# Kernel tuning notes

Measured on AMD Instinct MI355X. Metric: run time of the kernel, lower is better.

The kernel has to match this reference:

```python
import jax, jax.numpy as jnp
from jax import lax
import numpy as np

B, S, T = 64, 256, 256          # sentences, tokens, parser transitions per sentence
WDIMS, PDIMS = 128, 32
H = 256                          # per-direction hidden = ldims // 2
LDIMS = 2 * H
HID = 512
NRELS = 46
K, NNVECS = 3, 3
SLOTS = (K + 1) * NNVECS         # 12 gathered hidden vectors per transition
FEAT = LDIMS * SLOTS             # 6144 = hidLayer input dim
VW, VP = 40003, 53
ROUT = 2 * NRELS + 1             # 93


def _lstm(x, Wih, Whh, bih, bhh, reverse=False):
    """torch.nn.LSTMCell recurrence over seq axis. x: [B,S,D] -> h: [B,S,H]."""
    Bx = x.shape[0]
    Hh = Whh.shape[1]
    xs = jnp.swapaxes(x, 0, 1)  # [S,B,D]
    xg = xs @ Wih.T + (bih + bhh)  # precompute input gates [S,B,4H]

    def step(carry, g_in):
        h, c = carry
        g = g_in + h @ Whh.T
        i, f, gg, o = jnp.split(g, 4, axis=-1)
        i = jax.nn.sigmoid(i); f = jax.nn.sigmoid(f)
        gg = jnp.tanh(gg); o = jax.nn.sigmoid(o)
        c = f * c + i * gg
        h = o * jnp.tanh(c)
        return (h, c), h

    init = (jnp.zeros((Bx, Hh), x.dtype), jnp.zeros((Bx, Hh), x.dtype))
    _, hs = lax.scan(step, init, xg, reverse=reverse)
    return jnp.swapaxes(hs, 0, 1)  # [B,S,H], backward pass aligned to positions


def _forward(word_ids, pos_ids, feat_idx, wlookup, plookup,
             Wih1f, Whh1f, bih1f, bhh1f, Wih1b, Whh1b, bih1b, bhh1b,
             Wih2f, Whh2f, bih2f, bhh2f, Wih2b, Whh2b, bih2b, bhh2b,
             hidLayer, hidBias, outLayer, outBias,
             rhidLayer, rhidBias, routLayer, routBias):
    # token embeddings: ivec = cat(wordvec, posvec)
    ivec = jnp.concatenate([wlookup[word_ids], plookup[pos_ids]], axis=-1)  # [B,S,160]
    # first biLSTM
    f1 = _lstm(ivec, Wih1f, Whh1f, bih1f, bhh1f)
    b1 = _lstm(ivec, Wih1b, Whh1b, bih1b, bhh1b, reverse=True)
    vec1 = jnp.concatenate([f1, b1], axis=-1)  # [B,S,512]
    # second biLSTM (bibiFlag)
    f2 = _lstm(vec1, Wih2f, Whh2f, bih2f, bhh2f)
    b2 = _lstm(vec1, Wih2b, Whh2b, bih2b, bhh2b, reverse=True)
    vec = jnp.concatenate([f2, b2], axis=-1)  # [B,S,512]
    # __evaluate: concat (k+1)*nnvecs hidden vectors per transition
    bidx = jnp.arange(B)[:, None, None]
    feats = vec[bidx, feat_idx]                      # [B,T,12,512]
    feats = feats.reshape(B, T, FEAT)                # [B,T,6144]
    # unlabeled action scores: out = outLayer @ tanh(hidLayer @ input + hidBias) + outBias
    hid = jnp.tanh(jnp.einsum('btf,hf->bth', feats, hidLayer) + hidBias)
    out = jnp.einsum('bth,oh->bto', hid, outLayer) + outBias        # [B,T,3]
    # labeled relation scores
    rhid = jnp.tanh(jnp.einsum('btf,hf->bth', feats, rhidLayer) + rhidBias)
    rout = jnp.einsum('bth,oh->bto', rhid, routLayer) + routBias    # [B,T,93]
    return out, rout


def setup_inputs() -> dict:
    key = jax.random.key(0)
    ks = iter(jax.random.split(key, 40))

    def nrm(shape, scale=0.05):
        return jax.random.normal(next(ks), shape, jnp.float32) * scale

    inp = {}
    inp['word_ids'] = jax.random.randint(next(ks), (B, S), 0, VW)
    inp['pos_ids'] = jax.random.randint(next(ks), (B, S), 0, VP)
    inp['feat_idx'] = jax.random.randint(next(ks), (B, T, SLOTS), 0, S)
    inp['wlookup'] = nrm((VW, WDIMS))
    inp['plookup'] = nrm((VP, PDIMS))
    D1 = WDIMS + PDIMS
    for tag, din in (('1f', D1), ('1b', D1), ('2f', LDIMS), ('2b', LDIMS)):
        inp['Wih' + tag] = nrm((4 * H, din))
        inp['Whh' + tag] = nrm((4 * H, H))
        inp['bih' + tag] = nrm((4 * H,))
        inp['bhh' + tag] = nrm((4 * H,))
    inp['hidLayer'] = nrm((HID, FEAT), 0.02)
    inp['hidBias'] = nrm((HID,))
    inp['outLayer'] = nrm((3, HID))
    inp['outBias'] = nrm((3,))
    inp['rhidLayer'] = nrm((HID, FEAT), 0.02)
    inp['rhidBias'] = nrm((HID,))
    inp['routLayer'] = nrm((ROUT, HID))
    inp['routBias'] = nrm((ROUT,))
    return inp


def reference(word_ids, pos_ids, feat_idx, wlookup, plookup,
              Wih1f, Whh1f, bih1f, bhh1f, Wih1b, Whh1b, bih1b, bhh1b,
              Wih2f, Whh2f, bih2f, bhh2f, Wih2b, Whh2b, bih2b, bhh2b,
              hidLayer, hidBias, outLayer, outBias,
              rhidLayer, rhidBias, routLayer, routBias):
    return _forward(word_ids, pos_ids, feat_idx, wlookup, plookup,
                    Wih1f, Whh1f, bih1f, bhh1f, Wih1b, Whh1b, bih1b, bhh1b,
                    Wih2f, Whh2f, bih2f, bhh2f, Wih2b, Whh2b, bih2b, bhh2b,
                    hidLayer, hidBias, outLayer, outBias,
                    rhidLayer, rhidBias, routLayer, routBias)
```

## Files before the change

### kernel.cpp

```cpp
#include <hip/hip_runtime.h>
#include <hip/hip_fp16.h>
#include <math.h>


namespace {
constexpr int kB = 64, kS = 256, kH = 256, kG4 = 1024;
constexpr int kLD = 512;
constexpr int kTok = kB * kS;
}

typedef _Float16 h2 __attribute__((ext_vector_type(2)));
typedef _Float16 h4 __attribute__((ext_vector_type(4)));
typedef _Float16 h8 __attribute__((ext_vector_type(8)));
typedef float f4 __attribute__((ext_vector_type(4)));

#if __has_builtin(__builtin_amdgcn_fdot2)
#define USE_FDOT2 1
#else
#define USE_FDOT2 0
#endif

__device__ __forceinline__ float dot2acc(h2 w, h2 hh, float acc) {
#if USE_FDOT2
  return __builtin_amdgcn_fdot2(w, hh, acc, false);
#else
  return fmaf((float)w.x, (float)hh.x, fmaf((float)w.y, (float)hh.y, acc));
#endif
}

__device__ __forceinline__ float fastrcp(float x) {
#if __has_builtin(__builtin_amdgcn_rcpf)
  return __builtin_amdgcn_rcpf(x);
#else
  return 1.f / x;
#endif
}
__device__ __forceinline__ float sigf(float x) { return fastrcp(1.f + __expf(-x)); }
__device__ __forceinline__ float tanhfast(float x) {
  float u = __expf(2.f * x);
  return 1.f - 2.f * fastrcp(u + 1.f);
}

__device__ __forceinline__ void stage16(const void* g, void* lds_base, int lane) {
#if __has_builtin(__builtin_amdgcn_global_load_lds)
  (void)lane;
  __builtin_amdgcn_global_load_lds((const __attribute__((address_space(1))) void*)g,
                                   (__attribute__((address_space(3))) void*)lds_base,
                                   16, 0, 0);
#else
  *(uint4*)((char*)lds_base + lane * 16) = *(const uint4*)g;
#endif
}

__global__ void embed_h(const int* __restrict__ wid, const int* __restrict__ pid,
                        const float* __restrict__ wl, const float* __restrict__ pl,
                        _Float16* __restrict__ dst) {
  int tid = blockIdx.x * blockDim.x + threadIdx.x;
  if (tid >= kTok * 24) return;
  int tok = tid / 24, c8 = tid % 24;
  h8 o;
  if (c8 < 20) {
    const float* src = (c8 < 16) ? (wl + (size_t)wid[tok] * 128 + c8 * 8)
                                 : (pl + (size_t)pid[tok] * 32 + (c8 - 16) * 8);
    float4 v0 = *(const float4*)src;
    float4 v1 = *(const float4*)(src + 4);
    o[0] = (_Float16)v0.x; o[1] = (_Float16)v0.y;
    o[2] = (_Float16)v0.z; o[3] = (_Float16)v0.w;
    o[4] = (_Float16)v1.x; o[5] = (_Float16)v1.y;
    o[6] = (_Float16)v1.z; o[7] = (_Float16)v1.w;
  } else {
    o = (h8)(_Float16)0.f;
  }
  *(h8*)(dst + (size_t)tok * 192 + c8 * 8) = o;
}

__global__ void f2h_pad(const float* __restrict__ src, _Float16* __restrict__ dst,
                        int rows, int Kin, int Kpad) {
  int per = Kpad >> 2;
  int tid = blockIdx.x * blockDim.x + threadIdx.x;
  if (tid >= rows * per) return;
  int row = tid / per, c4 = (tid % per) << 2;
  h4 o;
  if (c4 < Kin) {
    float4 v = *(const float4*)(src + (size_t)row * Kin + c4);
    o[0] = (_Float16)v.x; o[1] = (_Float16)v.y;
    o[2] = (_Float16)v.z; o[3] = (_Float16)v.w;
  } else {
    o = (h4)(_Float16)0.f;
  }
  *(h4*)(dst + (size_t)row * Kpad + c4) = o;
}

__global__ void prep_bias(const float* __restrict__ b0, const float* __restrict__ b1,
                          const float* __restrict__ b2, const float* __restrict__ b3,
                          const float* __restrict__ b4, const float* __restrict__ b5,
                          const float* __restrict__ b6, const float* __restrict__ b7,
                          float* __restrict__ bsum) {
  int tid = blockIdx.x * blockDim.x + threadIdx.x;
  if (tid >= 4 * kG4) return;
  int grp = tid >> 10, i = tid & 1023;
  const float* x; const float* y;
  switch (grp) {
    case 0: x = b0; y = b1; break;
    case 1: x = b2; y = b3; break;
    case 2: x = b4; y = b5; break;
    default: x = b6; y = b7; break;
  }
  bsum[tid] = x[i] + y[i];
}

__global__ void concat_bias(const float* __restrict__ a, const float* __restrict__ b,
                            float* __restrict__ dst) {
  int tid = blockIdx.x * blockDim.x + threadIdx.x;
  if (tid >= kG4) return;
  dst[tid] = (tid < 512) ? a[tid] : b[tid - 512];
}

template <bool GATHER, bool TANH>
__global__ __launch_bounds__(256) void mfma_gemm(
    const _Float16* __restrict__ A, int lda,
    const _Float16* __restrict__ W,
    const float* __restrict__ bias,
    const _Float16* __restrict__ vsrc, const int* __restrict__ fidx,
    float* __restrict__ C, int K) {
  __shared__ _Float16 Asm[128 * 64];
  __shared__ _Float16 Bsm[128 * 64];
  const int tid = threadIdx.x;
  const int w = tid >> 6, l = tid & 63;
  const int wr = w >> 1, wc = w & 1;
  const int m0 = blockIdx.y * 128, n0 = blockIdx.x * 128;
  const int lrow = l & 15, lk8 = (l >> 4) << 3;
  const int stg_r = l >> 3;
  const int stg_c = (l & 7) ^ stg_r;

  f4 acc[4][4] = {};

  for (int k0 = 0; k0 < K; k0 += 64) {
#pragma unroll
    for (int ii = 0; ii < 4; ++ii) {
      const int r = w * 32 + ii * 8 + stg_r;
      const _Float16* ga;
      if (GATHER) {
        const int token = m0 + r;
        const int slot = k0 >> 9;
        const int idx = fidx[token * 12 + slot];
        ga = vsrc + ((((size_t)(token >> 8) << 8) + idx) << 9) + (k0 & 511) + (stg_c << 3);
      } else {
        ga = A + (size_t)(m0 + r) * lda + k0 + (stg_c << 3);
      }
      stage16(ga, &Asm[(size_t)(w * 32 + ii * 8) * 64], l);
      const _Float16* gb = W + (size_t)(n0 + r) * K + k0 + (stg_c << 3);
      stage16(gb, &Bsm[(size_t)(w * 32 + ii * 8) * 64], l);
    }
    __syncthreads();
#pragma unroll
    for (int kk = 0; kk < 64; kk += 32) {
      const int c0 = (kk + lk8) >> 3;
      h8 af[4], bf[4];
#pragma unroll
      for (int m = 0; m < 4; ++m) {
        const int row = wr * 64 + m * 16 + lrow;
        af[m] = *(const h8*)&Asm[row * 64 + ((c0 ^ (row & 7)) << 3)];
      }
#pragma unroll
      for (int n = 0; n < 4; ++n) {
        const int row = wc * 64 + n * 16 + lrow;
        bf[n] = *(const h8*)&Bsm[row * 64 + ((c0 ^ (row & 7)) << 3)];
      }
#pragma unroll
      for (int m = 0; m < 4; ++m)
#pragma unroll
        for (int n = 0; n < 4; ++n)
          acc[m][n] = __builtin_amdgcn_mfma_f32_16x16x32_f16(af[m], bf[n], acc[m][n], 0, 0, 0);
    }
    __syncthreads();
  }
#pragma unroll
  for (int n = 0; n < 4; ++n) {
    const int col = n0 + wc * 64 + n * 16 + lrow;
    const float bb = bias[col];
#pragma unroll
    for (int m = 0; m < 4; ++m) {
      const int rowb = m0 + wr * 64 + m * 16 + ((l >> 4) << 2);
#pragma unroll
      for (int r = 0; r < 4; ++r) {
        float v = acc[m][n][r] + bb;
        if (TANH) v = tanhf(v);
        C[(size_t)(rowb + r) * kG4 + col] = v;
      }
    }
  }
}

template <bool TANH>
__global__ __launch_bounds__(256) void gemm_kernel(
    const float* __restrict__ A, int lda,
    const float* __restrict__ W,
    const float* __restrict__ bias,
    float* __restrict__ C, int ldc, int N, int K) {
  __shared__ float As[8][128];
  __shared__ float Bs[8][128];
  const int tid = threadIdx.x;
  const int m0 = blockIdx.y * 128;
  const int n0 = blockIdx.x * 128;
  const int tx = tid & 15, ty = tid >> 4;
  const int lm = tid >> 1;
  const int lk = (tid & 1) * 4;
  float acc[8][8] = {};

  for (int k0 = 0; k0 < K; k0 += 8) {
    float4 av = *(const float4*)(A + (size_t)(m0 + lm) * lda + k0 + lk);
    const int n = n0 + lm;
    float4 bv = make_float4(0.f, 0.f, 0.f, 0.f);
    if (n < N) bv = *(const float4*)(W + (size_t)n * K + k0 + lk);
    __syncthreads();
    As[lk + 0][lm] = av.x; As[lk + 1][lm] = av.y;
    As[lk + 2][lm] = av.z; As[lk + 3][lm] = av.w;
    Bs[lk + 0][lm] = bv.x; Bs[lk + 1][lm] = bv.y;
    Bs[lk + 2][lm] = bv.z; Bs[lk + 3][lm] = bv.w;
    __syncthreads();
#pragma unroll
    for (int kk = 0; kk < 8; kk++) {
      float a[8], b8[8];
      *(float4*)&a[0]  = *(const float4*)&As[kk][ty * 8];
      *(float4*)&a[4]  = *(const float4*)&As[kk][ty * 8 + 4];
      *(float4*)&b8[0] = *(const float4*)&Bs[kk][tx * 8];
      *(float4*)&b8[4] = *(const float4*)&Bs[kk][tx * 8 + 4];
#pragma unroll
      for (int i = 0; i < 8; i++)
#pragma unroll
        for (int j = 0; j < 8; j++)
          acc[i][j] = fmaf(a[i], b8[j], acc[i][j]);
    }
  }
#pragma unroll
  for (int i = 0; i < 8; i++) {
    size_t m = m0 + ty * 8 + i;
#pragma unroll
    for (int j = 0; j < 8; j++) {
      int n = n0 + tx * 8 + j;
      if (n < N) {
        float v = acc[i][j] + bias[n];
        if (TANH) v = tanhf(v);
        C[m * ldc + n] = v;
      }
    }
  }
}

__global__ __launch_bounds__(512, 2) void lstm_rec_kernel(
    const float* __restrict__ xg_f, const float* __restrict__ xg_b,
    const float* __restrict__ Whh_f, const float* __restrict__ Whh_b,
    _Float16* __restrict__ out ) {
  __shared__ uint4 wlds4[16 * 512];
  __shared__ __align__(16) _Float16 hbuf[2][kH];

  const int bid = blockIdx.x;
  const int dir = bid & 1;
  const int row = bid >> 1;
  const float* xg  = dir ? xg_b : xg_f;
  const float* Whh = dir ? Whh_b : Whh_f;
  const int t = threadIdx.x;
  const int c  = t >> 1;
  const int kh = t & 1;
  const int kbase = kh * 128;

  h2 wv[4][48];
#pragma unroll
  for (int g = 0; g < 4; ++g) {
    const float2* wr = (const float2*)(Whh + (size_t)(g * kH + c) * kH + kbase);
#pragma unroll
    for (int p = 0; p < 48; ++p) {
      float2 f = wr[p];
      h2 a; a.x = (_Float16)f.x; a.y = (_Float16)f.y;
      wv[g][p] = a;
    }
#pragma unroll
    for (int q = 0; q < 4; ++q) {
      unsigned u[4];
#pragma unroll
      for (int i = 0; i < 4; ++i) {
        float2 f = wr[48 + 4 * q + i];
        h2 a; a.x = (_Float16)f.x; a.y = (_Float16)f.y;
        u[i] = __builtin_bit_cast(unsigned, a);
      }
      wlds4[(g * 4 + q) * 512 + t] = make_uint4(u[0], u[1], u[2], u[3]);
    }
  }
  if (t < kH) hbuf[1][t] = (_Float16)0.f;
  float c_state = 0.f;
  __syncthreads();

  const float* xgr = xg + (size_t)(row * kS) * kG4;
  const int sstep = dir ? -1 : 1;
  int s = dir ? (kS - 1) : 0;
  float x0 = xgr[(size_t)s * kG4 + c];
  float x1 = xgr[(size_t)s * kG4 + c + 256];
  float x2 = xgr[(size_t)s * kG4 + c + 512];
  float x3 = xgr[(size_t)s * kG4 + c + 768];

  for (int it = 0; it < kS; ++it) {
    int sn = s + sstep; sn = sn < 0 ? 0 : (sn > kS - 1 ? kS - 1 : sn);
    const float* xnrow = xgr + (size_t)sn * kG4 + c;
    float xn0 = xnrow[0], xn1 = xnrow[256], xn2 = xnrow[512], xn3 = xnrow[768];

    float a0 = kh ? 0.f : x0;
    float a1 = kh ? 0.f : x1;
    float a2 = kh ? 0.f : x2;
    float a3 = kh ? 0.f : x3;

    const uint4* hh = ((const uint4*)hbuf[(it & 1) ^ 1]) + kh * 16;
#pragma unroll
    for (int u = 0; u < 12; ++u) {
      uint4 hv = hh[u];
      h2 h0 = __builtin_bit_cast(h2, hv.x);
      h2 h1 = __builtin_bit_cast(h2, hv.y);
      h2 hx = __builtin_bit_cast(h2, hv.z);
      h2 h3 = __builtin_bit_cast(h2, hv.w);
      a0 = dot2acc(wv[0][4*u+0], h0, a0); a0 = dot2acc(wv[0][4*u+1], h1, a0);
      a0 = dot2acc(wv[0][4*u+2], hx, a0); a0 = dot2acc(wv[0][4*u+3], h3, a0);
      a1 = dot2acc(wv[1][4*u+0], h0, a1); a1 = dot2acc(wv[1][4*u+1], h1, a1);
      a1 = dot2acc(wv[1][4*u+2], hx, a1); a1 = dot2acc(wv[1][4*u+3], h3, a1);
      a2 = dot2acc(wv[2][4*u+0], h0, a2); a2 = dot2acc(wv[2][4*u+1], h1, a2);
      a2 = dot2acc(wv[2][4*u+2], hx, a2); a2 = dot2acc(wv[2][4*u+3], h3, a2);
      a3 = dot2acc(wv[3][4*u+0], h0, a3); a3 = dot2acc(wv[3][4*u+1], h1, a3);
      a3 = dot2acc(wv[3][4*u+2], hx, a3); a3 = dot2acc(wv[3][4*u+3], h3, a3);
    }
#pragma unroll
    for (int q = 0; q < 4; ++q) {
      uint4 hv = hh[12 + q];
      h2 h0 = __builtin_bit_cast(h2, hv.x);
      h2 h1 = __builtin_bit_cast(h2, hv.y);
      h2 hx = __builtin_bit_cast(h2, hv.z);
      h2 h3 = __builtin_bit_cast(h2, hv.w);
      uint4 w0 = wlds4[(0 * 4 + q) * 512 + t];
      uint4 w1 = wlds4[(1 * 4 + q) * 512 + t];
      uint4 w2 = wlds4[(2 * 4 + q) * 512 + t];
      uint4 w3 = wlds4[(3 * 4 + q) * 512 + t];
      a0 = dot2acc(__builtin_bit_cast(h2, w0.x), h0, a0);
      a0 = dot2acc(__builtin_bit_cast(h2, w0.y), h1, a0);
      a0 = dot2acc(__builtin_bit_cast(h2, w0.z), hx, a0);
      a0 = dot2acc(__builtin_bit_cast(h2, w0.w), h3, a0);
      a1 = dot2acc(__builtin_bit_cast(h2, w1.x), h0, a1);
      a1 = dot2acc(__builtin_bit_cast(h2, w1.y), h1, a1);
      a1 = dot2acc(__builtin_bit_cast(h2, w1.z), hx, a1);
      a1 = dot2acc(__builtin_bit_cast(h2, w1.w), h3, a1);
      a2 = dot2acc(__builtin_bit_cast(h2, w2.x), h0, a2);
      a2 = dot2acc(__builtin_bit_cast(h2, w2.y), h1, a2);
      a2 = dot2acc(__builtin_bit_cast(h2, w2.z), hx, a2);
      a2 = dot2acc(__builtin_bit_cast(h2, w2.w), h3, a2);
      a3 = dot2acc(__builtin_bit_cast(h2, w3.x), h0, a3);
      a3 = dot2acc(__builtin_bit_cast(h2, w3.y), h1, a3);
      a3 = dot2acc(__builtin_bit_cast(h2, w3.z), hx, a3);
      a3 = dot2acc(__builtin_bit_cast(h2, w3.w), h3, a3);
    }
    float s0 = a0 + __shfl_xor(a0, 1);
    float s1 = a1 + __shfl_xor(a1, 1);
    float s2 = a2 + __shfl_xor(a2, 1);
    float s3 = a3 + __shfl_xor(a3, 1);
    float i_ = sigf(s0);
    float f_ = sigf(s1);
    float g_ = tanhfast(s2);
    float o_ = sigf(s3);
    c_state = f_ * c_state + i_ * g_;
    float h = o_ * tanhfast(c_state);
    if (!kh) {
      hbuf[it & 1][c] = (_Float16)h;
      out[((size_t)(row * kS + s)) * kLD + dir * kH + c] = (_Float16)h;
    }
    s += sstep;
    __syncthreads();
    x0 = xn0; x1 = xn1; x2 = xn2; x3 = xn3;
  }
}

extern "C" void kernel_launch(void* const* d_in, const int* in_sizes, int n_in,
                              void* d_out, int out_size, void* d_ws, size_t ws_size,
                              hipStream_t stream) {
  const int*   word_ids = (const int*)d_in[0];
  const int*   pos_ids  = (const int*)d_in[1];
  const int*   feat_idx = (const int*)d_in[2];
  const float* wlookup  = (const float*)d_in[3];
  const float* plookup  = (const float*)d_in[4];
  const float* Wih1f = (const float*)d_in[5];
  const float* Whh1f = (const float*)d_in[6];
  const float* bih1f = (const float*)d_in[7];
  const float* bhh1f = (const float*)d_in[8];
  const float* Wih1b = (const float*)d_in[9];
  const float* Whh1b = (const float*)d_in[10];
  const float* bih1b = (const float*)d_in[11];
  const float* bhh1b = (const float*)d_in[12];
  const float* Wih2f = (const float*)d_in[13];
  const float* Whh2f = (const float*)d_in[14];
  const float* bih2f = (const float*)d_in[15];
  const float* bhh2f = (const float*)d_in[16];
  const float* Wih2b = (const float*)d_in[17];
  const float* Whh2b = (const float*)d_in[18];
  const float* bih2b = (const float*)d_in[19];
  const float* bhh2b = (const float*)d_in[20];
  const float* hidLayer  = (const float*)d_in[21];
  const float* hidBias   = (const float*)d_in[22];
  const float* outLayer  = (const float*)d_in[23];
  const float* outBias   = (const float*)d_in[24];
  const float* rhidLayer = (const float*)d_in[25];
  const float* rhidBias  = (const float*)d_in[26];
  const float* routLayer = (const float*)d_in[27];
  const float* routBias  = (const float*)d_in[28];

  float* ws = (float*)d_ws;
  const size_t F_IVECH = 0;
  const size_t F_XGF   = F_IVECH + (size_t)kTok * 192 / 2;
  const size_t F_XGB   = F_XGF + (size_t)kTok * kG4;
  const size_t F_V1H   = F_XGB + (size_t)kTok * kG4;
  const size_t F_V2H   = F_V1H + (size_t)kTok * kLD / 2;
  const size_t F_WHA   = F_V2H + (size_t)kTok * kLD / 2;
  const size_t F_WHB   = F_WHA + (size_t)2 * kG4 * 192 / 2;
  const size_t F_WHID  = F_WHB + (size_t)2 * kG4 * 512 / 2;
  const size_t F_BSUM  = F_WHID + (size_t)kG4 * 6144 / 2;
  const size_t F_HB    = F_BSUM + 4 * kG4;
  const size_t F_END   = F_HB + kG4;
  const size_t F_HID   = F_XGF;
  if (ws_size < F_END * sizeof(float)) return;

  _Float16* ivec_h = (_Float16*)(ws + F_IVECH);
  float*    xg_f   = ws + F_XGF;
  float*    xg_b   = ws + F_XGB;
  _Float16* vec1h  = (_Float16*)(ws + F_V1H);
  _Float16* vec2h  = (_Float16*)(ws + F_V2H);
  _Float16* whA    = (_Float16*)(ws + F_WHA);
  _Float16* whB    = (_Float16*)(ws + F_WHB);
  _Float16* whid   = (_Float16*)(ws + F_WHID);
  float*    bsum   = ws + F_BSUM;
  float*    hb     = ws + F_HB;
  float*    hidc   = ws + F_HID;
  float*    outp   = (float*)d_out;

  prep_bias<<<16, 256, 0, stream>>>(bih1f, bhh1f, bih1b, bhh1b,
                                    bih2f, bhh2f, bih2b, bhh2b, bsum);
  concat_bias<<<4, 256, 0, stream>>>(hidBias, rhidBias, hb);
  f2h_pad<<<(1024 * 48 + 255) / 256, 256, 0, stream>>>(Wih1f, whA, 1024, 160, 192);
  f2h_pad<<<(1024 * 48 + 255) / 256, 256, 0, stream>>>(Wih1b, whA + 1024 * 192, 1024, 160, 192);
  f2h_pad<<<(1024 * 128 + 255) / 256, 256, 0, stream>>>(Wih2f, whB, 1024, 512, 512);
  f2h_pad<<<(1024 * 128 + 255) / 256, 256, 0, stream>>>(Wih2b, whB + 1024 * 512, 1024, 512, 512);
  f2h_pad<<<(512 * 1536 + 255) / 256, 256, 0, stream>>>(hidLayer, whid, 512, 6144, 6144);
  f2h_pad<<<(512 * 1536 + 255) / 256, 256, 0, stream>>>(rhidLayer, whid + (size_t)512 * 6144,
                                                        512, 6144, 6144);
  embed_h<<<(kTok * 24 + 255) / 256, 256, 0, stream>>>(word_ids, pos_ids,
                                                       wlookup, plookup, ivec_h);
  mfma_gemm<false, false><<<dim3(8, 128), 256, 0, stream>>>(
      ivec_h, 192, whA, bsum + 0, nullptr, nullptr, xg_f, 192);
  mfma_gemm<false, false><<<dim3(8, 128), 256, 0, stream>>>(
      ivec_h, 192, whA + 1024 * 192, bsum + 1024, nullptr, nullptr, xg_b, 192);
  lstm_rec_kernel<<<128, 512, 0, stream>>>(xg_f, xg_b, Whh1f, Whh1b, vec1h);
  mfma_gemm<false, false><<<dim3(8, 128), 256, 0, stream>>>(
      vec1h, 512, whB, bsum + 2048, nullptr, nullptr, xg_f, 512);
  mfma_gemm<false, false><<<dim3(8, 128), 256, 0, stream>>>(
      vec1h, 512, whB + 1024 * 512, bsum + 3072, nullptr, nullptr, xg_b, 512);
  lstm_rec_kernel<<<128, 512, 0, stream>>>(xg_f, xg_b, Whh2f, Whh2b, vec2h);
  mfma_gemm<true, true><<<dim3(8, 128), 256, 0, stream>>>(
      nullptr, 0, whid, hb, vec2h, feat_idx, hidc, 6144);
  gemm_kernel<false><<<dim3(1, 128), 256, 0, stream>>>(
      hidc, kG4, outLayer, outBias, outp, 3, 3, 512);
  gemm_kernel<false><<<dim3(1, 128), 256, 0, stream>>>(
      hidc + 512, kG4, routLayer, routBias, outp + (size_t)kTok * 3, 93, 93, 512);
}
```

Before: 1.663 ms.

## Interleave gate layout, fp16 hidden output, fuse output heads into one MFMA GEMM

The input-gate GEMMs now write gates interleaved per hidden unit, so each recurrence thread loads its four gate values with one float4 instead of four strided loads. The cross-lane pair reduction uses a DPP move instead of a shuffle. The hidden layer writes fp16 tanh output, and both output heads are packed into one zero-padded 96-column fp16 weight matrix. That matrix is consumed by the MFMA GEMM, replacing two fp32 SIMT GEMMs. This trades extra padded K work and fp16 rounding on the hidden activations for fewer launches and tensor-core use.

Result: no change. 1.641 ms (-1.3%).

```diff
diff --git a/kernel.cpp b/kernel.cpp
--- a/kernel.cpp
+++ b/kernel.cpp
@@ -39,6 +39,15 @@
 __device__ __forceinline__ float tanhfast(float x) {
   float u = __expf(2.f * x);
   return 1.f - 2.f * fastrcp(u + 1.f);
+}
+
+__device__ __forceinline__ float dppadd1(float x) {
+#if __has_builtin(__builtin_amdgcn_mov_dpp)
+  int y = __builtin_amdgcn_mov_dpp(__builtin_bit_cast(int, x), 0xB1, 0xF, 0xF, true);
+  return x + __builtin_bit_cast(float, y);
+#else
+  return x + __shfl_xor(x, 1);
+#endif
 }
 
 __device__ __forceinline__ void stage16(const void* g, void* lds_base, int lane) {
@@ -116,13 +125,26 @@
   dst[tid] = (tid < 512) ? a[tid] : b[tid - 512];
 }
 
-template <bool GATHER, bool TANH>
+__global__ void build_w96(const float* __restrict__ outL, const float* __restrict__ outB,
+                          const float* __restrict__ routL, const float* __restrict__ routB,
+                          _Float16* __restrict__ w, float* __restrict__ b) {
+  int tid = blockIdx.x * blockDim.x + threadIdx.x;
+  if (tid >= 128 * 1024) return;
+  int n = tid >> 10, k = tid & 1023;
+  float v = 0.f;
+  if (n < 3) { if (k < 512) v = outL[n * 512 + k]; }
+  else if (n < 96) { if (k >= 512) v = routL[(size_t)(n - 3) * 512 + (k - 512)]; }
+  w[tid] = (_Float16)v;
+  if (k == 0) b[n] = (n < 3) ? outB[n] : (n < 96 ? routB[n - 3] : 0.f);
+}
+
+template <bool GATHER, int CMODE>
 __global__ __launch_bounds__(256) void mfma_gemm(
     const _Float16* __restrict__ A, int lda,
     const _Float16* __restrict__ W,
     const float* __restrict__ bias,
     const _Float16* __restrict__ vsrc, const int* __restrict__ fidx,
-    float* __restrict__ C, int K) {
+    void* __restrict__ C, int K) {
   __shared__ _Float16 Asm[128 * 64];
   __shared__ _Float16 Bsm[128 * 64];
   const int tid = threadIdx.x;
@@ -185,64 +207,17 @@
 #pragma unroll
       for (int r = 0; r < 4; ++r) {
         float v = acc[m][n][r] + bb;
-        if (TANH) v = tanhf(v);
-        C[(size_t)(rowb + r) * kG4 + col] = v;
-      }
-    }
-  }
-}
-
-template <bool TANH>
-__global__ __launch_bounds__(256) void gemm_kernel(
-    const float* __restrict__ A, int lda,
-    const float* __restrict__ W,
-    const float* __restrict__ bias,
-    float* __restrict__ C, int ldc, int N, int K) {
-  __shared__ float As[8][128];
-  __shared__ float Bs[8][128];
-  const int tid = threadIdx.x;
-  const int m0 = blockIdx.y * 128;
-  const int n0 = blockIdx.x * 128;
-  const int tx = tid & 15, ty = tid >> 4;
-  const int lm = tid >> 1;
-  const int lk = (tid & 1) * 4;
-  float acc[8][8] = {};
-
-  for (int k0 = 0; k0 < K; k0 += 8) {
-    float4 av = *(const float4*)(A + (size_t)(m0 + lm) * lda + k0 + lk);
-    const int n = n0 + lm;
-    float4 bv = make_float4(0.f, 0.f, 0.f, 0.f);
-    if (n < N) bv = *(const float4*)(W + (size_t)n * K + k0 + lk);
-    __syncthreads();
-    As[lk + 0][lm] = av.x; As[lk + 1][lm] = av.y;
-    As[lk + 2][lm] = av.z; As[lk + 3][lm] = av.w;
-    Bs[lk + 0][lm] = bv.x; Bs[lk + 1][lm] = bv.y;
-    Bs[lk + 2][lm] = bv.z; Bs[lk + 3][lm] = bv.w;
-    __syncthreads();
-#pragma unroll
-    for (int kk = 0; kk < 8; kk++) {
-      float a[8], b8[8];
-      *(float4*)&a[0]  = *(const float4*)&As[kk][ty * 8];
-      *(float4*)&a[4]  = *(const float4*)&As[kk][ty * 8 + 4];
-      *(float4*)&b8[0] = *(const float4*)&Bs[kk][tx * 8];
-      *(float4*)&b8[4] = *(const float4*)&Bs[kk][tx * 8 + 4];
-#pragma unroll
-      for (int i = 0; i < 8; i++)
-#pragma unroll
-        for (int j = 0; j < 8; j++)
-          acc[i][j] = fmaf(a[i], b8[j], acc[i][j]);
-    }
-  }
-#pragma unroll
-  for (int i = 0; i < 8; i++) {
-    size_t m = m0 + ty * 8 + i;
-#pragma unroll
-    for (int j = 0; j < 8; j++) {
-      int n = n0 + tx * 8 + j;
-      if (n < N) {
-        float v = acc[i][j] + bias[n];
-        if (TANH) v = tanhf(v);
-        C[m * ldc + n] = v;
+        const size_t row = rowb + r;
+        if (CMODE == 0) {
+          ((float*)C)[row * kG4 + col] = v;
+        } else if (CMODE == 1) {
+          ((float*)C)[row * kG4 + ((col & 255) * 4 + (col >> 8))] = v;
+        } else if (CMODE == 2) {
+          ((_Float16*)C)[row * kG4 + col] = (_Float16)tanhf(v);
+        } else {
+          if (col < 3)       ((float*)C)[row * 3 + col] = v;
+          else if (col < 96) ((float*)C)[(size_t)kTok * 3 + row * 93 + (col - 3)] = v;
+        }
       }
     }
   }
@@ -294,20 +269,16 @@
   const float* xgr = xg + (size_t)(row * kS) * kG4;
   const int sstep = dir ? -1 : 1;
   int s = dir ? (kS - 1) : 0;
-  float x0 = xgr[(size_t)s * kG4 + c];
-  float x1 = xgr[(size_t)s * kG4 + c + 256];
-  float x2 = xgr[(size_t)s * kG4 + c + 512];
-  float x3 = xgr[(size_t)s * kG4 + c + 768];
+  float4 xv = *(const float4*)(xgr + (size_t)s * kG4 + 4 * c);
 
   for (int it = 0; it < kS; ++it) {
     int sn = s + sstep; sn = sn < 0 ? 0 : (sn > kS - 1 ? kS - 1 : sn);
-    const float* xnrow = xgr + (size_t)sn * kG4 + c;
-    float xn0 = xnrow[0], xn1 = xnrow[256], xn2 = xnrow[512], xn3 = xnrow[768];
-
-    float a0 = kh ? 0.f : x0;
-    float a1 = kh ? 0.f : x1;
-    float a2 = kh ? 0.f : x2;
-    float a3 = kh ? 0.f : x3;
+    float4 xvn = *(const float4*)(xgr + (size_t)sn * kG4 + 4 * c);
+
+    float a0 = kh ? 0.f : xv.x;
+    float a1 = kh ? 0.f : xv.y;
+    float a2 = kh ? 0.f : xv.z;
+    float a3 = kh ? 0.f : xv.w;
 
     const uint4* hh = ((const uint4*)hbuf[(it & 1) ^ 1]) + kh * 16;
 #pragma unroll
@@ -354,10 +325,10 @@
       a3 = dot2acc(__builtin_bit_cast(h2, w3.z), hx, a3);
       a3 = dot2acc(__builtin_bit_cast(h2, w3.w), h3, a3);
     }
-    float s0 = a0 + __shfl_xor(a0, 1);
-    float s1 = a1 + __shfl_xor(a1, 1);
-    float s2 = a2 + __shfl_xor(a2, 1);
-    float s3 = a3 + __shfl_xor(a3, 1);
+    float s0 = dppadd1(a0);
+    float s1 = dppadd1(a1);
+    float s2 = dppadd1(a2);
+    float s3 = dppadd1(a3);
     float i_ = sigf(s0);
     float f_ = sigf(s1);
     float g_ = tanhfast(s2);
@@ -370,7 +341,7 @@
     }
     s += sstep;
     __syncthreads();
-    x0 = xn0; x1 = xn1; x2 = xn2; x3 = xn3;
+    xv = xvn;
   }
 }
 
@@ -418,13 +389,15 @@
   const size_t F_WHID  = F_WHB + (size_t)2 * kG4 * 512 / 2;
   const size_t F_BSUM  = F_WHID + (size_t)kG4 * 6144 / 2;
   const size_t F_HB    = F_BSUM + 4 * kG4;
-  const size_t F_END   = F_HB + kG4;
+  const size_t F_W96   = F_HB + kG4;
+  const size_t F_B96   = F_W96 + (size_t)128 * kG4 / 2;
+  const size_t F_END   = F_B96 + 128;
   const size_t F_HID   = F_XGF;
   if (ws_size < F_END * sizeof(float)) return;
 
   _Float16* ivec_h = (_Float16*)(ws + F_IVECH);
-  float*    xg_f   = ws + F_XGF;
-  float*    xg_b   = ws + F_XGB;
+  float*    xgs_f  = ws + F_XGF;
+  float*    xgs_b  = ws + F_XGB;
   _Float16* vec1h  = (_Float16*)(ws + F_V1H);
   _Float16* vec2h  = (_Float16*)(ws + F_V2H);
   _Float16* whA    = (_Float16*)(ws + F_WHA);
@@ -432,12 +405,15 @@
   _Float16* whid   = (_Float16*)(ws + F_WHID);
   float*    bsum   = ws + F_BSUM;
   float*    hb     = ws + F_HB;
-  float*    hidc   = ws + F_HID;
+  _Float16* w96    = (_Float16*)(ws + F_W96);
+  float*    b96    = ws + F_B96;
+  _Float16* hidc_h = (_Float16*)(ws + F_HID);
   float*    outp   = (float*)d_out;
 
   prep_bias<<<16, 256, 0, stream>>>(bih1f, bhh1f, bih1b, bhh1b,
                                     bih2f, bhh2f, bih2b, bhh2b, bsum);
   concat_bias<<<4, 256, 0, stream>>>(hidBias, rhidBias, hb);
+  build_w96<<<512, 256, 0, stream>>>(outLayer, outBias, routLayer, routBias, w96, b96);
   f2h_pad<<<(1024 * 48 + 255) / 256, 256, 0, stream>>>(Wih1f, whA, 1024, 160, 192);
   f2h_pad<<<(1024 * 48 + 255) / 256, 256, 0, stream>>>(Wih1b, whA + 1024 * 192, 1024, 160, 192);
   f2h_pad<<<(1024 * 128 + 255) / 256, 256, 0, stream>>>(Wih2f, whB, 1024, 512, 512);
@@ -447,20 +423,18 @@
                                                         512, 6144, 6144);
   embed_h<<<(kTok * 24 + 255) / 256, 256, 0, stream>>>(word_ids, pos_ids,
                                                        wlookup, plookup, ivec_h);
-  mfma_gemm<false, false><<<dim3(8, 128), 256, 0, stream>>>(
-      ivec_h, 192, whA, bsum + 0, nullptr, nullptr, xg_f, 192);
-  mfma_gemm<false, false><<<dim3(8, 128), 256, 0, stream>>>(
-      ivec_h, 192, whA + 1024 * 192, bsum + 1024, nullptr, nullptr, xg_b, 192);
-  lstm_rec_kernel<<<128, 512, 0, stream>>>(xg_f, xg_b, Whh1f, Whh1b, vec1h);
-  mfma_gemm<false, false><<<dim3(8, 128), 256, 0, stream>>>(
-      vec1h, 512, whB, bsum + 2048, nullptr, nullptr, xg_f, 512);
-  mfma_gemm<false, false><<<dim3(8, 128), 256, 0, stream>>>(
-      vec1h, 512, whB + 1024 * 512, bsum + 3072, nullptr, nullptr, xg_b, 512);
-  lstm_rec_kernel<<<128, 512, 0, stream>>>(xg_f, xg_b, Whh2f, Whh2b, vec2h);
-  mfma_gemm<true, true><<<dim3(8, 128), 256, 0, stream>>>(
-      nullptr, 0, whid, hb, vec2h, feat_idx, hidc, 6144);
-  gemm_kernel<false><<<dim3(1, 128), 256, 0, stream>>>(
-      hidc, kG4, outLayer, outBias, outp, 3, 3, 512);
-  gemm_kernel<false><<<dim3(1, 128), 256, 0, stream>>>(
-      hidc + 512, kG4, routLayer, routBias, outp + (size_t)kTok * 3, 93, 93, 512);
-}
+  mfma_gemm<false, 1><<<dim3(8, 128), 256, 0, stream>>>(
+      ivec_h, 192, whA, bsum + 0, nullptr, nullptr, xgs_f, 192);
+  mfma_gemm<false, 1><<<dim3(8, 128), 256, 0, stream>>>(
+      ivec_h, 192, whA + 1024 * 192, bsum + 1024, nullptr, nullptr, xgs_b, 192);
+  lstm_rec_kernel<<<128, 512, 0, stream>>>(xgs_f, xgs_b, Whh1f, Whh1b, vec1h);
+  mfma_gemm<false, 1><<<dim3(8, 128), 256, 0, stream>>>(
+      vec1h, 512, whB, bsum + 2048, nullptr, nullptr, xgs_f, 512);
+  mfma_gemm<false, 1><<<dim3(8, 128), 256, 0, stream>>>(
+      vec1h, 512, whB + 1024 * 512, bsum + 3072, nullptr, nullptr, xgs_b, 512);
+  lstm_rec_kernel<<<128, 512, 0, stream>>>(xgs_f, xgs_b, Whh2f, Whh2b, vec2h);
+  mfma_gemm<true, 2><<<dim3(8, 128), 256, 0, stream>>>(
+      nullptr, 0, whid, hb, vec2h, feat_idx, hidc_h, 6144);
+  mfma_gemm<false, 3><<<dim3(1, 128), 256, 0, stream>>>(
+      hidc_h, kG4, w96, b96, nullptr, nullptr, outp, kG4);
+}
```
